# Kernel tuning notes

Hardware: AMD Instinct MI355X
Metric: run time of the kernel (lower is better)

## Reference

```python
import jax, jax.numpy as jnp
import numpy as np

N_NODES = 100000
IN_FEATS = 256
N_EDGES = 3200000
N_SEL = 4096
J_POOL = 50  # eval branch: inner loop over first 50 selected nodes


def setup_inputs() -> dict:
    key = jax.random.key(0)
    ks = jax.random.split(key, 16)
    x = jax.random.normal(ks[0], (N_NODES, IN_FEATS), dtype=jnp.float32)
    edge_index = jax.random.randint(ks[1], (2, N_EDGES), 0, N_NODES)
    nodes = jax.random.randint(ks[2], (N_SEL,), 0, N_NODES)
    s1 = 1.0 / np.sqrt(IN_FEATS)
    s2 = 1.0 / np.sqrt(32)
    s3 = 1.0 / np.sqrt(16)
    return {
        "x": x,
        "w1": jax.random.uniform(ks[3], (IN_FEATS, 32), jnp.float32, -s1, s1),
        "b1": jnp.zeros((32,), jnp.float32),
        "w2": jax.random.uniform(ks[4], (32, 16), jnp.float32, -s2, s2),
        "b2": jnp.zeros((16,), jnp.float32),
        "gate1_w": jax.random.normal(ks[5], (32, 4), jnp.float32) * 0.02,
        "e1_w": jax.random.uniform(ks[6], (4, 32, 16), jnp.float32, -s2, s2),
        "e1_b": jnp.zeros((4, 16), jnp.float32),
        "gate2_w": jax.random.normal(ks[7], (16, 4), jnp.float32) * 0.02,
        "e2_w": jax.random.uniform(ks[8], (4, 16, 2), jnp.float32, -s3, s3),
        "e2_b": jnp.zeros((4, 2), jnp.float32),
        "edge_index": edge_index,
        "nodes": nodes,
    }


def _gcn_conv(h, w, b, src, dst, n):
    hw = h @ w
    deg = jnp.zeros((n,), hw.dtype).at[dst].add(1.0)
    dis = jax.lax.rsqrt(jnp.maximum(deg, 1e-12))
    norm = dis[src] * dis[dst]
    msg = hw[src] * norm[:, None]
    return jax.ops.segment_sum(msg, dst, num_segments=n) + b


def _moe_top1(z, gate_w, ew, eb):
    # k=1 gating: softmax over a single selected logit == weight 1.0
    idx = jnp.argmax(z @ gate_w, axis=-1)              # [M]
    outs = jnp.einsum('mi,eio->meo', z, ew) + eb        # [M, E, O]
    return jnp.take_along_axis(outs, idx[:, None, None], axis=1)[:, 0]


def reference(x, w1, b1, w2, b2, gate1_w, e1_w, e1_b, gate2_w, e2_w, e2_b,
              edge_index, nodes):
    n = x.shape[0]
    loops = jnp.arange(n)
    src = jnp.concatenate([edge_index[0], loops])
    dst = jnp.concatenate([edge_index[1], loops])

    h = jax.nn.relu(_gcn_conv(x, w1, b1, src, dst, n))   # dropout: eval mode (identity)
    h = _gcn_conv(h, w2, b2, src, dst, n)                # [N, 16]

    # eval branch pairwise concat: i over all selected nodes, j over first 50
    hi = jnp.repeat(h[nodes], J_POOL, axis=0)            # [M, 16]
    hj = jnp.tile(h[nodes[:J_POOL]], (nodes.shape[0], 1))  # [M, 16]
    x_sim = jnp.concatenate([hi, hj], axis=-1)           # [M, 32]

    z = jax.nn.relu(_moe_top1(x_sim, gate1_w, e1_w, e1_b))
    z = _moe_top1(z, gate2_w, e2_w, e2_b)                # [M, 2]
    return jax.nn.log_softmax(z, axis=1), x_sim
```

## Files before the change

### kernel.cpp

```cpp
#include <hip/hip_runtime.h>
#include <hip/hip_fp16.h>
#include <math.h>


#define NPB 64
#define NB_PAD 2048
#define BATCH 8192
#define NSCAP 12288

__global__ void zero_kernel(int* __restrict__ p, int c) {
    int i = blockIdx.x * 256 + threadIdx.x;
    if (i < c) p[i] = 0;
}

__global__ __launch_bounds__(256) void histA_kernel(const int* __restrict__ ei,
                                                    int* __restrict__ bhist, int nE, int nb) {
    __shared__ int h[NB_PAD];
    int tid = threadIdx.x;
    for (int t = tid; t < nb; t += 256) h[t] = 0;
    __syncthreads();
    int base = blockIdx.x * 4096;
    for (int t = tid; t < 4096; t += 256) {
        int e = base + t;
        if (e < nE) atomicAdd(&h[ei[nE + e] >> 6], 1);
    }
    __syncthreads();
    for (int t = tid; t < nb; t += 256) { int c = h[t]; if (c) atomicAdd(&bhist[t], c); }
}

__global__ __launch_bounds__(256) void scanB_kernel(const int* __restrict__ bhist,
                                                    int* __restrict__ boffs,
                                                    int* __restrict__ gcur, int nb) {
    int t = threadIdx.x;
    int v[8], s = 0;
    #pragma unroll
    for (int i = 0; i < 8; ++i) { int c = t * 8 + i; v[i] = (c < nb) ? bhist[c] : 0; s += v[i]; }
    int lane = t & 63, wid = t >> 6;
    int incl = s;
    for (int d = 1; d < 64; d <<= 1) { int u = __shfl_up(incl, (unsigned)d, 64); if (lane >= d) incl += u; }
    __shared__ int ws[4];
    if (lane == 63) ws[wid] = incl;
    __syncthreads();
    int add = 0;
    for (int w = 0; w < wid; ++w) add += ws[w];
    incl += add;
    int excl = incl - s;
    #pragma unroll
    for (int i = 0; i < 8; ++i) {
        int c = t * 8 + i;
        if (c < nb) { boffs[c] = excl; gcur[c] = excl; }
        excl += v[i];
    }
    if (t == 0) boffs[nb] = ws[0] + ws[1] + ws[2] + ws[3];
}

__global__ __launch_bounds__(256) void scatterC_kernel(const int* __restrict__ ei,
                                                       int* __restrict__ gcur,
                                                       int* __restrict__ keys, int nE, int nb) {
    __shared__ int kbuf[BATCH];
    __shared__ unsigned short kbk[BATCH];
    __shared__ int lstart[NB_PAD];
    __shared__ int cursor[NB_PAD];
    __shared__ int gbase[NB_PAD];
    __shared__ int ws2[4];
    int tid = threadIdx.x;
    int base = blockIdx.x * BATCH;
    int cnt = nE - base; if (cnt > BATCH) cnt = BATCH;
    for (int t = tid; t < nb; t += 256) lstart[t] = 0;
    __syncthreads();
    for (int t = tid; t < cnt; t += 256)
        atomicAdd(&lstart[ei[nE + base + t] >> 6], 1);
    __syncthreads();
    {
        int v[8], s = 0;
        #pragma unroll
        for (int i = 0; i < 8; ++i) { int c = tid * 8 + i; v[i] = (c < nb) ? lstart[c] : 0; s += v[i]; }
        int lane = tid & 63, wid = tid >> 6;
        int incl = s;
        for (int d = 1; d < 64; d <<= 1) { int u = __shfl_up(incl, (unsigned)d, 64); if (lane >= d) incl += u; }
        if (lane == 63) ws2[wid] = incl;
        __syncthreads();
        int add = 0;
        for (int w = 0; w < wid; ++w) add += ws2[w];
        incl += add;
        int excl = incl - s;
        #pragma unroll
        for (int i = 0; i < 8; ++i) {
            int c = tid * 8 + i;
            if (c < nb) { lstart[c] = excl; cursor[c] = excl; }
            excl += v[i];
        }
    }
    __syncthreads();
    for (int t = tid; t < nb; t += 256) {
        int e = (t == nb - 1) ? cnt : lstart[t + 1];
        int c = e - lstart[t];
        gbase[t] = c ? atomicAdd(&gcur[t], c) : 0;
    }
    for (int t = tid; t < cnt; t += 256) {
        int d = ei[nE + base + t];
        int s = ei[base + t];
        int b = d >> 6;
        int pos = atomicAdd(&cursor[b], 1);
        kbuf[pos] = s | ((d & 63) << 17);
        kbk[pos] = (unsigned short)b;
    }
    __syncthreads();
    for (int j = tid; j < cnt; j += 256) {
        int b = kbk[j];
        keys[gbase[b] + (j - lstart[b])] = kbuf[j];
    }
}

__global__ __launch_bounds__(256) void nodesort_kernel(int* __restrict__ keys,
                                                       const int* __restrict__ boffs,
                                                       int* __restrict__ noffs,
                                                       float* __restrict__ dis,
                                                       int n, int nbuck) {
    __shared__ int kb[NSCAP];
    __shared__ int cnt[NPB], cur[NPB];
    int tid = threadIdx.x, b = blockIdx.x;
    int off = boffs[b], end = boffs[b + 1];
    int m = end - off; if (m > NSCAP) m = NSCAP;
    if (tid < NPB) cnt[tid] = 0;
    __syncthreads();
    for (int t = tid; t < m; t += 256) {
        int k = keys[off + t];
        kb[t] = k;
        atomicAdd(&cnt[k >> 17], 1);
    }
    __syncthreads();
    if (tid < NPB) {
        int v = cnt[tid];
        int incl = v;
        for (int d = 1; d < 64; d <<= 1) { int u = __shfl_up(incl, (unsigned)d, 64); if (tid >= d) incl += u; }
        int excl = incl - v;
        cur[tid] = excl;
        int node = b * NPB + tid;
        if (node < n) {
            noffs[node] = off + excl;
            dis[node] = rsqrtf((float)(v + 1));
        }
    }
    __syncthreads();
    for (int t = tid; t < m; t += 256) {
        int k = kb[t];
        int pos = atomicAdd(&cur[k >> 17], 1);
        keys[off + pos] = k & 0x1FFFF;
    }
    if (b == nbuck - 1 && tid == 0) noffs[n] = end;
}

__global__ __launch_bounds__(256) void hw1s_kernel(const float* __restrict__ x,
                                                   const float* __restrict__ w1,
                                                   const float* __restrict__ dis,
                                                   __half* __restrict__ hw1h, int n) {
    __shared__ float xs[32 * 258];
    __shared__ float w1s[32 * 32];
    int tid = threadIdx.x;
    int row0 = blockIdx.x * 256;
    int rt = tid & 31, kt = tid >> 5;
    float acc[8][4];
    #pragma unroll
    for (int i = 0; i < 8; ++i) {
        #pragma unroll
        for (int j = 0; j < 4; ++j) acc[i][j] = 0.f;
    }

    for (int ch = 0; ch < 8; ++ch) {
        int cc0 = ch * 32;
        __syncthreads();
        #pragma unroll
        for (int i = 0; i < 8; ++i) {
            int gid = i * 256 + tid;
            int r = gid >> 3, c4 = (gid & 7) << 2;
            int row = row0 + r;
            float4 v = (row < n) ? *(const float4*)&x[(size_t)row * 256 + cc0 + c4]
                                 : make_float4(0.f, 0.f, 0.f, 0.f);
            xs[(c4 + 0) * 258 + r] = v.x;
            xs[(c4 + 1) * 258 + r] = v.y;
            xs[(c4 + 2) * 258 + r] = v.z;
            xs[(c4 + 3) * 258 + r] = v.w;
        }
        {
            int c = tid >> 3, k4 = (tid & 7) << 2;
            *(float4*)&w1s[c * 32 + k4] = *(const float4*)&w1[(size_t)(cc0 + c) * 32 + k4];
        }
        __syncthreads();
        #pragma unroll 4
        for (int c = 0; c < 32; ++c) {
            float4 wv = *(float4*)&w1s[c * 32 + kt * 4];
            float xv[8];
            #pragma unroll
            for (int i = 0; i < 8; ++i) xv[i] = xs[c * 258 + rt + 32 * i];
            #pragma unroll
            for (int i = 0; i < 8; ++i) {
                acc[i][0] = fmaf(xv[i], wv.x, acc[i][0]);
                acc[i][1] = fmaf(xv[i], wv.y, acc[i][1]);
                acc[i][2] = fmaf(xv[i], wv.z, acc[i][2]);
                acc[i][3] = fmaf(xv[i], wv.w, acc[i][3]);
            }
        }
    }
    #pragma unroll
    for (int i = 0; i < 8; ++i) {
        int row = row0 + rt + 32 * i;
        if (row < n) {
            float dn = dis[row];
            __half2 h01 = __floats2half2_rn(acc[i][0] * dn, acc[i][1] * dn);
            __half2 h23 = __floats2half2_rn(acc[i][2] * dn, acc[i][3] * dn);
            __half2* dst = (__half2*)&hw1h[(size_t)row * 32 + kt * 4];
            dst[0] = h01; dst[1] = h23;
        }
    }
}

__global__ __launch_bounds__(256) void gatherG1_kernel(const __half* __restrict__ hw1h,
                                                       const float* __restrict__ dis,
                                                       const int* __restrict__ srcs,
                                                       const int* __restrict__ noffs,
                                                       const float* __restrict__ b1,
                                                       __half* __restrict__ h1h, int n) {
    int tid = threadIdx.x;
    int g = tid >> 5, k = tid & 31;
    int node = blockIdx.x * 8 + g;
    if (node >= n) return;
    int off = noffs[node], end = noffs[node + 1];
    float acc = 0.f;
    int e = off;
    for (; e + 8 <= end; e += 8) {
        int s0 = srcs[e],     s1 = srcs[e + 1], s2 = srcs[e + 2], s3 = srcs[e + 3];
        int s4 = srcs[e + 4], s5 = srcs[e + 5], s6 = srcs[e + 6], s7 = srcs[e + 7];
        float v0 = __half2float(hw1h[(size_t)s0 * 32 + k]);
        float v1 = __half2float(hw1h[(size_t)s1 * 32 + k]);
        float v2 = __half2float(hw1h[(size_t)s2 * 32 + k]);
        float v3 = __half2float(hw1h[(size_t)s3 * 32 + k]);
        float v4 = __half2float(hw1h[(size_t)s4 * 32 + k]);
        float v5 = __half2float(hw1h[(size_t)s5 * 32 + k]);
        float v6 = __half2float(hw1h[(size_t)s6 * 32 + k]);
        float v7 = __half2float(hw1h[(size_t)s7 * 32 + k]);
        acc += ((v0 + v1) + (v2 + v3)) + ((v4 + v5) + (v6 + v7));
    }
    for (; e < end; ++e)
        acc += __half2float(hw1h[(size_t)srcs[e] * 32 + k]);
    float dn = dis[node];
    float self = __half2float(hw1h[(size_t)node * 32 + k]);
    float h = fmaxf(dn * (acc + self) + b1[k], 0.f);
    h1h[(size_t)node * 32 + k] = __float2half(h);
}

__global__ __launch_bounds__(256) void gemm2_kernel(const __half* __restrict__ h1h,
                                                    const float* __restrict__ w2,
                                                    const float* __restrict__ dis,
                                                    float* __restrict__ hw2s, int n) {
    __shared__ float w2s[512];
    __shared__ float h1s[16][33];
    int tid = threadIdx.x;
    for (int t = tid; t < 512; t += 256) w2s[t] = w2[t];
    int node0 = blockIdx.x * 16;
    for (int t = tid; t < 512; t += 256) {
        int r = t >> 5, c = t & 31;
        int nd = node0 + r;
        h1s[r][c] = (nd < n) ? __half2float(h1h[(size_t)nd * 32 + c]) : 0.f;
    }
    __syncthreads();
    int r = tid >> 4, j = tid & 15;
    int nd = node0 + r;
    if (nd < n) {
        float a = 0.f;
        #pragma unroll
        for (int c = 0; c < 32; ++c) a += h1s[r][c] * w2s[c * 16 + j];
        hw2s[(size_t)nd * 16 + j] = a * dis[nd];
    }
}

__global__ __launch_bounds__(256) void gatherG2_kernel(const float* __restrict__ hw2s,
                                                       const float* __restrict__ dis,
                                                       const int* __restrict__ srcs,
                                                       const int* __restrict__ noffs,
                                                       const int* __restrict__ nodes,
                                                       const float* __restrict__ b2,
                                                       float* __restrict__ h2, int nsel, int n) {
    int tid = threadIdx.x;
    int slot = tid >> 4, j = tid & 15;
    int i = blockIdx.x * 16 + slot;
    if (i >= nsel) return;
    int node = nodes[i];
    int off = noffs[node], end = noffs[node + 1];
    float acc = 0.f;
    int e = off;
    for (; e + 4 <= end; e += 4) {
        int s0 = srcs[e], s1 = srcs[e + 1], s2 = srcs[e + 2], s3 = srcs[e + 3];
        float v0 = hw2s[(size_t)s0 * 16 + j];
        float v1 = hw2s[(size_t)s1 * 16 + j];
        float v2 = hw2s[(size_t)s2 * 16 + j];
        float v3 = hw2s[(size_t)s3 * 16 + j];
        acc += (v0 + v1) + (v2 + v3);
    }
    for (; e < end; ++e) acc += hw2s[(size_t)srcs[e] * 16 + j];
    h2[(size_t)node * 16 + j] = dis[node] * (acc + hw2s[(size_t)node * 16 + j]) + b2[j];
}

__global__ __launch_bounds__(256) void pair_moe_kernel(const float* __restrict__ h2,
                                                       const int* __restrict__ nodes,
                                                       const float* __restrict__ gate1_w,
                                                       const float* __restrict__ e1_w,
                                                       const float* __restrict__ e1_b,
                                                       const float* __restrict__ gate2_w,
                                                       const float* __restrict__ e2_w,
                                                       const float* __restrict__ e2_b,
                                                       float* __restrict__ out1,
                                                       float* __restrict__ out2, int M) {
    __shared__ float hjs[50 * 16];
    __shared__ float g1s[32 * 4];
    __shared__ float e1ws[4 * 32 * 16];
    __shared__ float e1bs[4 * 16];
    __shared__ float g2s[16 * 4];
    __shared__ float e2ws[4 * 16 * 2];
    __shared__ float e2bs[4 * 2];
    int tid = threadIdx.x;
    for (int t = tid; t < 800; t += 256) { int j = t >> 4, c = t & 15; hjs[t] = h2[nodes[j] * 16 + c]; }
    for (int t = tid; t < 128; t += 256) g1s[t] = gate1_w[t];
    for (int t = tid; t < 2048; t += 256) e1ws[t] = e1_w[t];
    for (int t = tid; t < 64; t += 256) e1bs[t] = e1_b[t];
    for (int t = tid; t < 64; t += 256) g2s[t] = gate2_w[t];
    for (int t = tid; t < 128; t += 256) e2ws[t] = e2_w[t];
    if (tid < 8) e2bs[tid] = e2_b[tid];
    __syncthreads();

    int m = blockIdx.x * 256 + tid;
    if (m >= M) return;
    int i = m / 50, j = m - i * 50;

    float xs[32];
    int ni = nodes[i];
    float4 a0 = *(const float4*)&h2[ni * 16];
    float4 a1 = *(const float4*)&h2[ni * 16 + 4];
    float4 a2 = *(const float4*)&h2[ni * 16 + 8];
    float4 a3 = *(const float4*)&h2[ni * 16 + 12];
    xs[0]=a0.x; xs[1]=a0.y; xs[2]=a0.z; xs[3]=a0.w;
    xs[4]=a1.x; xs[5]=a1.y; xs[6]=a1.z; xs[7]=a1.w;
    xs[8]=a2.x; xs[9]=a2.y; xs[10]=a2.z; xs[11]=a2.w;
    xs[12]=a3.x; xs[13]=a3.y; xs[14]=a3.z; xs[15]=a3.w;
    #pragma unroll
    for (int c = 0; c < 16; ++c) xs[16 + c] = hjs[j * 16 + c];

    #pragma unroll
    for (int c = 0; c < 32; c += 4)
        *(float4*)&out2[(size_t)m * 32 + c] = make_float4(xs[c], xs[c+1], xs[c+2], xs[c+3]);

    float g[4] = {0.f, 0.f, 0.f, 0.f};
    #pragma unroll
    for (int c = 0; c < 32; ++c) {
        float xv = xs[c];
        #pragma unroll
        for (int e = 0; e < 4; ++e) g[e] += xv * g1s[c * 4 + e];
    }
    int idx = 0; float best = g[0];
    #pragma unroll
    for (int e = 1; e < 4; ++e) if (g[e] > best) { best = g[e]; idx = e; }
    float z[16];
    #pragma unroll
    for (int o = 0; o < 16; ++o) {
        float a = e1bs[idx * 16 + o];
        #pragma unroll
        for (int c = 0; c < 32; ++c) a += xs[c] * e1ws[(idx * 32 + c) * 16 + o];
        z[o] = fmaxf(a, 0.f);
    }

    float g2[4] = {0.f, 0.f, 0.f, 0.f};
    #pragma unroll
    for (int c = 0; c < 16; ++c) {
        float zv = z[c];
        #pragma unroll
        for (int e = 0; e < 4; ++e) g2[e] += zv * g2s[c * 4 + e];
    }
    int idx2 = 0; float best2 = g2[0];
    #pragma unroll
    for (int e = 1; e < 4; ++e) if (g2[e] > best2) { best2 = g2[e]; idx2 = e; }
    float z2[2];
    #pragma unroll
    for (int o = 0; o < 2; ++o) {
        float a = e2bs[idx2 * 2 + o];
        #pragma unroll
        for (int c = 0; c < 16; ++c) a += z[c] * e2ws[(idx2 * 16 + c) * 2 + o];
        z2[o] = a;
    }

    float mx = fmaxf(z2[0], z2[1]);
    float l = logf(expf(z2[0] - mx) + expf(z2[1] - mx));
    out1[(size_t)m * 2 + 0] = z2[0] - mx - l;
    out1[(size_t)m * 2 + 1] = z2[1] - mx - l;
}

extern "C" void kernel_launch(void* const* d_in, const int* in_sizes, int n_in,
                              void* d_out, int out_size, void* d_ws, size_t ws_size,
                              hipStream_t stream) {
    const float* x       = (const float*)d_in[0];
    const float* w1      = (const float*)d_in[1];
    const float* b1      = (const float*)d_in[2];
    const float* w2      = (const float*)d_in[3];
    const float* b2      = (const float*)d_in[4];
    const float* gate1_w = (const float*)d_in[5];
    const float* e1_w    = (const float*)d_in[6];
    const float* e1_b    = (const float*)d_in[7];
    const float* gate2_w = (const float*)d_in[8];
    const float* e2_w    = (const float*)d_in[9];
    const float* e2_b    = (const float*)d_in[10];
    const int*   ei      = (const int*)d_in[11];
    const int*   nodes   = (const int*)d_in[12];

    const int n    = in_sizes[0] / 256;
    const int nE   = in_sizes[11] / 2;
    const int nsel = in_sizes[12];
    const int M    = nsel * 50;
    const int nb   = (n + NPB - 1) / NPB;

    size_t off = 0;
    auto alloc = [&](size_t bytes) -> void* {
        void* p = (char*)d_ws + off;
        off += (bytes + 255) & ~(size_t)255;
        return p;
    };
    float*  dis    = (float*)alloc((size_t)n * 4);
    int*    bhist  = (int*)alloc((size_t)nb * 4);
    int*    boffs  = (int*)alloc((size_t)(nb + 1) * 4);
    int*    gcur   = (int*)alloc((size_t)nb * 4);
    int*    noffs  = (int*)alloc((size_t)(n + 1) * 4);
    int*    keys   = (int*)alloc((size_t)nE * 4);
    __half* hw1h   = (__half*)alloc((size_t)n * 32 * 2);
    __half* h1h    = (__half*)alloc((size_t)n * 32 * 2);
    float*  hw2s   = (float*)alloc((size_t)n * 16 * 4);
    float*  h2     = (float*)alloc((size_t)n * 16 * 4);
    if (off > ws_size) return;

    float* out1 = (float*)d_out;
    float* out2 = out1 + (size_t)M * 2;

    zero_kernel<<<(nb + 255) / 256, 256, 0, stream>>>(bhist, nb);
    histA_kernel<<<(nE + 4095) / 4096, 256, 0, stream>>>(ei, bhist, nE, nb);
    scanB_kernel<<<1, 256, 0, stream>>>(bhist, boffs, gcur, nb);
    scatterC_kernel<<<(nE + BATCH - 1) / BATCH, 256, 0, stream>>>(ei, gcur, keys, nE, nb);
    nodesort_kernel<<<nb, 256, 0, stream>>>(keys, boffs, noffs, dis, n, nb);
    hw1s_kernel<<<(n + 255) / 256, 256, 0, stream>>>(x, w1, dis, hw1h, n);
    gatherG1_kernel<<<(n + 7) / 8, 256, 0, stream>>>(hw1h, dis, keys, noffs, b1, h1h, n);
    gemm2_kernel<<<(n + 15) / 16, 256, 0, stream>>>(h1h, w2, dis, hw2s, n);
    gatherG2_kernel<<<(nsel + 15) / 16, 256, 0, stream>>>(hw2s, dis, keys, noffs, nodes, b2,
                                                          h2, nsel, n);
    pair_moe_kernel<<<(M + 255) / 256, 256, 0, stream>>>(h2, nodes, gate1_w, e1_w, e1_b,
                                                         gate2_w, e2_w, e2_b, out1, out2, M);
}
```

Baseline: 241.2 us.

## Restructure X·W1 GEMM to 128-row tiles with wave-uniform W1 scalar loads

```diff
diff --git a/kernel.cpp b/kernel.cpp
--- a/kernel.cpp
+++ b/kernel.cpp
@@ -155,63 +155,50 @@
                                                    const float* __restrict__ w1,
                                                    const float* __restrict__ dis,
                                                    __half* __restrict__ hw1h, int n) {
-    __shared__ float xs[32 * 258];
-    __shared__ float w1s[32 * 32];
-    int tid = threadIdx.x;
-    int row0 = blockIdx.x * 256;
-    int rt = tid & 31, kt = tid >> 5;
-    float acc[8][4];
-    #pragma unroll
-    for (int i = 0; i < 8; ++i) {
-        #pragma unroll
-        for (int j = 0; j < 4; ++j) acc[i][j] = 0.f;
-    }
+    __shared__ float xs[32 * 130];
+    int tid = threadIdx.x;
+    int row0 = blockIdx.x * 128;
+    int r = tid & 127;
+    int khs = __builtin_amdgcn_readfirstlane((tid >> 7) * 16);
+    float acc[16];
+    #pragma unroll
+    for (int k = 0; k < 16; ++k) acc[k] = 0.f;
 
     for (int ch = 0; ch < 8; ++ch) {
         int cc0 = ch * 32;
         __syncthreads();
         #pragma unroll
-        for (int i = 0; i < 8; ++i) {
+        for (int i = 0; i < 4; ++i) {
             int gid = i * 256 + tid;
-            int r = gid >> 3, c4 = (gid & 7) << 2;
-            int row = row0 + r;
+            int rr = gid >> 3, c4 = (gid & 7) << 2;
+            int row = row0 + rr;
             float4 v = (row < n) ? *(const float4*)&x[(size_t)row * 256 + cc0 + c4]
                                  : make_float4(0.f, 0.f, 0.f, 0.f);
-            xs[(c4 + 0) * 258 + r] = v.x;
-            xs[(c4 + 1) * 258 + r] = v.y;
-            xs[(c4 + 2) * 258 + r] = v.z;
-            xs[(c4 + 3) * 258 + r] = v.w;
-        }
-        {
-            int c = tid >> 3, k4 = (tid & 7) << 2;
-            *(float4*)&w1s[c * 32 + k4] = *(const float4*)&w1[(size_t)(cc0 + c) * 32 + k4];
+            xs[(c4 + 0) * 130 + rr] = v.x;
+            xs[(c4 + 1) * 130 + rr] = v.y;
+            xs[(c4 + 2) * 130 + rr] = v.z;
+            xs[(c4 + 3) * 130 + rr] = v.w;
         }
         __syncthreads();
         #pragma unroll 4
         for (int c = 0; c < 32; ++c) {
-            float4 wv = *(float4*)&w1s[c * 32 + kt * 4];
-            float xv[8];
+            float xv = xs[c * 130 + r];
+            const float* wrow = &w1[(size_t)(cc0 + c) * 32 + khs];
             #pragma unroll
-            for (int i = 0; i < 8; ++i) xv[i] = xs[c * 258 + rt + 32 * i];
-            #pragma unroll
-            for (int i = 0; i < 8; ++i) {
-                acc[i][0] = fmaf(xv[i], wv.x, acc[i][0]);
-                acc[i][1] = fmaf(xv[i], wv.y, acc[i][1]);
-                acc[i][2] = fmaf(xv[i], wv.z, acc[i][2]);
-                acc[i][3] = fmaf(xv[i], wv.w, acc[i][3]);
-            }
+            for (int k = 0; k < 16; ++k)
+                acc[k] = fmaf(xv, wrow[k], acc[k]);
         }
     }
-    #pragma unroll
-    for (int i = 0; i < 8; ++i) {
-        int row = row0 + rt + 32 * i;
-        if (row < n) {
-            float dn = dis[row];
-            __half2 h01 = __floats2half2_rn(acc[i][0] * dn, acc[i][1] * dn);
-            __half2 h23 = __floats2half2_rn(acc[i][2] * dn, acc[i][3] * dn);
-            __half2* dst = (__half2*)&hw1h[(size_t)row * 32 + kt * 4];
-            dst[0] = h01; dst[1] = h23;
-        }
+    int row = row0 + r;
+    if (row < n) {
+        float dn = dis[row];
+        __half2 h[8];
+        #pragma unroll
+        for (int k = 0; k < 8; ++k)
+            h[k] = __floats2half2_rn(acc[2 * k] * dn, acc[2 * k + 1] * dn);
+        float4* dst = (float4*)&hw1h[(size_t)row * 32 + khs];
+        dst[0] = *(float4*)&h[0];
+        dst[1] = *(float4*)&h[4];
     }
 }
 
@@ -442,7 +429,7 @@
     scanB_kernel<<<1, 256, 0, stream>>>(bhist, boffs, gcur, nb);
     scatterC_kernel<<<(nE + BATCH - 1) / BATCH, 256, 0, stream>>>(ei, gcur, keys, nE, nb);
     nodesort_kernel<<<nb, 256, 0, stream>>>(keys, boffs, noffs, dis, n, nb);
-    hw1s_kernel<<<(n + 255) / 256, 256, 0, stream>>>(x, w1, dis, hw1h, n);
+    hw1s_kernel<<<(n + 127) / 128, 256, 0, stream>>>(x, w1, dis, hw1h, n);
     gatherG1_kernel<<<(n + 7) / 8, 256, 0, stream>>>(hw1h, dis, keys, noffs, b1, h1h, n);
     gemm2_kernel<<<(n + 15) / 16, 256, 0, stream>>>(h1h, w2, dis, hw2s, n);
     gatherG2_kernel<<<(nsel + 15) / 16, 256, 0, stream>>>(hw2s, dis, keys, noffs, nodes, b2,
```

Result: faster. 229.0 us (-5.1%).
